# Kernel optimization log

Measured on AMD Instinct MI355X. Metric: run time of the kernel, lower is better.

The kernel has to match this reference:

```python
import jax, jax.numpy as jnp
import numpy as np

R, B, D = 1024, 16, 1024
K_ACTIVE = 20
FB_DECAY = 0.9          # feedback_decay
REFR_W = 1.0            # refractory_weight
FB_W = 0.5              # feedback_weight


def _hex_neighbors(rows=32, cols=32):
    """Toroidal hex grid adjacency: 6 neighbors per region, shape [R, 6]."""
    n = rows * cols
    idx = np.arange(n)
    r, c = idx // cols, idx % cols
    def wrap(rr, cc):
        return (rr % rows) * cols + (cc % cols)
    nbrs = np.stack([
        wrap(r, c - 1), wrap(r, c + 1),
        wrap(r - 1, c), wrap(r + 1, c),
        wrap(r - 1, c + 1), wrap(r + 1, c - 1),
    ], axis=1)
    return nbrs.astype(np.int32)


def setup_inputs() -> dict:
    key = jax.random.key(0)
    k1, k2, k3, k4, k5 = jax.random.split(key, 5)
    return {
        "H": jax.random.normal(k1, (R, B, D), jnp.float32),
        "neighbor_msg": jax.random.normal(k2, (R, B, D), jnp.float32),
        "w": jax.random.normal(k3, (D,), jnp.float32) / np.float32(np.sqrt(D)),
        "theta": jnp.zeros((R,), jnp.float32),
        "refractory": jax.random.uniform(k4, (B, R), jnp.float32),
        "feedback": jax.random.uniform(k5, (B, R), jnp.float32),
        "neighbor_indices": jnp.asarray(_hex_neighbors()),
    }


def _greedy_hex_nms(adj, nbrs, k):
    """adj: [B, R] adjusted scores; nbrs: [R, 6]. Returns hard mask [B, R]."""
    n_regions = adj.shape[1]

    def nms_one(scores):
        order = jnp.argsort(-scores)  # descending

        def step(state, idx):
            sel, sup, cnt = state
            take = (cnt < k) & (~sel[idx]) & (~sup[idx])
            sel = sel.at[idx].set(sel[idx] | take)
            sup = sup.at[idx].set(sup[idx] | take)
            nb = nbrs[idx]  # [6]
            sup = sup.at[nb].set(sup[nb] | take)
            return (sel, sup, cnt + take.astype(jnp.int32)), None

        init = (jnp.zeros(n_regions, bool), jnp.zeros(n_regions, bool), jnp.int32(0))
        (sel, _, _), _ = jax.lax.scan(step, init, order)
        return sel.astype(scores.dtype)

    return jax.vmap(nms_one)(adj)


def reference(H, neighbor_msg, w, theta, refractory, feedback, neighbor_indices):
    # learned score: Linear(D, 1, bias=False) -> [B, R]
    s = jnp.einsum('rbd,d->br', H, w)
    # feedback inhibition from routed message magnitude
    fb_mag = jnp.linalg.norm(neighbor_msg, axis=-1).T          # [B, R]
    fb_new = FB_DECAY * feedback + (1.0 - FB_DECAY) * fb_mag   # updated _feedback
    adj = s - theta[None, :] - REFR_W * refractory - FB_W * fb_new
    hard = jax.lax.stop_gradient(_greedy_hex_nms(adj, neighbor_indices, K_ACTIVE))
    soft = jax.nn.sigmoid(adj)
    ste = hard + soft - jax.lax.stop_gradient(soft)            # straight-through
    Hs = H * ste.T[:, :, None]                                 # [R, B, D]
    return Hs, hard, adj
```

## Files before the change

### kernel.cpp

```cpp
#include <hip/hip_runtime.h>
#include <hip/hip_bf16.h>
#include <math.h>

#define RR 1024
#define BB 16
#define DD 1024
#define K_ACTIVE 20

typedef float vfloat4 __attribute__((ext_vector_type(4)));

__global__ __launch_bounds__(256) void score_kernel(
    const float* __restrict__ H, const float* __restrict__ msg,
    const float* __restrict__ w, const float* __restrict__ theta,
    const float* __restrict__ refr, const float* __restrict__ fb,
    float* __restrict__ adj_out)
{
    const int wave = threadIdx.x >> 6;
    const int lane = threadIdx.x & 63;
    const int pair = blockIdx.x * 4 + wave;
    const int r = pair >> 4;
    const int b = pair & 15;

    const vfloat4* __restrict__ H4 = (const vfloat4*)(H + (size_t)pair * DD);
    const vfloat4* __restrict__ M4 = (const vfloat4*)(msg + (size_t)pair * DD);
    const vfloat4* __restrict__ W4 = (const vfloat4*)w;

    const vfloat4 h0 = H4[lane],       h1 = H4[lane + 64];
    const vfloat4 h2 = H4[lane + 128], h3 = H4[lane + 192];
    const vfloat4 m0 = M4[lane],       m1 = M4[lane + 64];
    const vfloat4 m2 = M4[lane + 128], m3 = M4[lane + 192];
    const vfloat4 w0 = W4[lane],       w1 = W4[lane + 64];
    const vfloat4 w2 = W4[lane + 128], w3 = W4[lane + 192];

    float dot = h0.x * w0.x + h0.y * w0.y + h0.z * w0.z + h0.w * w0.w;
    dot += h1.x * w1.x + h1.y * w1.y + h1.z * w1.z + h1.w * w1.w;
    dot += h2.x * w2.x + h2.y * w2.y + h2.z * w2.z + h2.w * w2.w;
    dot += h3.x * w3.x + h3.y * w3.y + h3.z * w3.z + h3.w * w3.w;

    float ss = m0.x * m0.x + m0.y * m0.y + m0.z * m0.z + m0.w * m0.w;
    ss += m1.x * m1.x + m1.y * m1.y + m1.z * m1.z + m1.w * m1.w;
    ss += m2.x * m2.x + m2.y * m2.y + m2.z * m2.z + m2.w * m2.w;
    ss += m3.x * m3.x + m3.y * m3.y + m3.z * m3.z + m3.w * m3.w;

#pragma unroll
    for (int off = 32; off > 0; off >>= 1) {
        dot += __shfl_down(dot, off);
        ss  += __shfl_down(ss, off);
    }
    if (lane == 0) {
        const float fb_mag = sqrtf(ss);
        const float fb_new = 0.9f * fb[b * RR + r] + 0.1f * fb_mag;
        adj_out[b * RR + r] = dot - theta[r] - refr[b * RR + r] - 0.5f * fb_new;
    }
}

__global__ __launch_bounds__(64) void nms_kernel(
    const float* __restrict__ adj, const int* __restrict__ nbrs,
    float* __restrict__ hard)
{
    __shared__ float val[RR];
    __shared__ int   nb[RR * 6];
    __shared__ unsigned char sel[RR];

    const int b = blockIdx.x;
    const int lane = threadIdx.x;

#pragma unroll
    for (int j = 0; j < 16; ++j) {
        const int i = lane + 64 * j;
        val[i] = adj[b * RR + i];
        sel[i] = 0;
    }
    const int4* nb4g = (const int4*)nbrs;
    int4* nb4s = (int4*)nb;
#pragma unroll
    for (int j = 0; j < 24; ++j)
        nb4s[lane + 64 * j] = nb4g[lane + 64 * j];
    __syncthreads();

    for (int it = 0; it < K_ACTIVE; ++it) {
        float m = -INFINITY;
        int mi = RR;
#pragma unroll
        for (int j = 0; j < 16; ++j) {
            const int i = lane + 64 * j;
            const float v = val[i];
            if (v > m || (v == m && i < mi)) { m = v; mi = i; }
        }
#pragma unroll
        for (int off = 32; off > 0; off >>= 1) {
            const float ov = __shfl_down(m, off);
            const int   oi = __shfl_down(mi, off);
            if (ov > m || (ov == m && oi < mi)) { m = ov; mi = oi; }
        }
        const int   bi = __shfl(mi, 0);
        const float bm = __shfl(m, 0);
        if (bm > -INFINITY) {
            if (lane == 0) { sel[bi] = 1; val[bi] = -INFINITY; }
            if (lane < 6)  { val[nb[bi * 6 + lane]] = -INFINITY; }
        }
        __syncthreads();
    }

#pragma unroll
    for (int j = 0; j < 16; ++j) {
        const int i = lane + 64 * j;
        hard[b * RR + i] = sel[i] ? 1.0f : 0.0f;
    }
}

__global__ __launch_bounds__(256) void gate_kernel(
    const float* __restrict__ H, const float* __restrict__ hard,
    float* __restrict__ Hs)
{
    const int wave = threadIdx.x >> 6;
    const int lane = threadIdx.x & 63;
    const int pair = blockIdx.x * 4 + wave;
    const int r = pair >> 4;
    const int b = pair & 15;
    const float g = hard[b * RR + r];

    vfloat4* out4 = (vfloat4*)(Hs + (size_t)pair * DD);
    if (g != 0.0f) {
        const vfloat4* H4 = (const vfloat4*)(H + (size_t)pair * DD);
        const vfloat4 v0 = H4[lane],       v1 = H4[lane + 64];
        const vfloat4 v2 = H4[lane + 128], v3 = H4[lane + 192];
        __builtin_nontemporal_store(v0, &out4[lane]);
        __builtin_nontemporal_store(v1, &out4[lane + 64]);
        __builtin_nontemporal_store(v2, &out4[lane + 128]);
        __builtin_nontemporal_store(v3, &out4[lane + 192]);
    } else {
        const vfloat4 z = {0.f, 0.f, 0.f, 0.f};
        __builtin_nontemporal_store(z, &out4[lane]);
        __builtin_nontemporal_store(z, &out4[lane + 64]);
        __builtin_nontemporal_store(z, &out4[lane + 128]);
        __builtin_nontemporal_store(z, &out4[lane + 192]);
    }
}

extern "C" void kernel_launch(void* const* d_in, const int* in_sizes, int n_in,
                              void* d_out, int out_size, void* d_ws, size_t ws_size,
                              hipStream_t stream) {
    const float* H     = (const float*)d_in[0];
    const float* msg   = (const float*)d_in[1];
    const float* w     = (const float*)d_in[2];
    const float* theta = (const float*)d_in[3];
    const float* refr  = (const float*)d_in[4];
    const float* fb    = (const float*)d_in[5];
    const int*   nbrs  = (const int*)d_in[6];

    float* out  = (float*)d_out;
    float* Hs   = out;
    float* hard = out + (size_t)RR * BB * DD;
    float* adj  = hard + (size_t)BB * RR;

    score_kernel<<<RR * BB / 4, 256, 0, stream>>>(H, msg, w, theta, refr, fb, adj);
    nms_kernel<<<BB, 64, 0, stream>>>(adj, nbrs, hard);
    gate_kernel<<<RR * BB / 4, 256, 0, stream>>>(H, hard, Hs);
}
```

Baseline: 209.9 us.

## Fuse score, NMS and gate kernels into one persistent kernel with grid barriers

Replaces three kernel launches with a single persistent kernel of 1024 blocks, each wave handling four (r,b) pairs. Software grid barriers built from atomic counters separate the score, NMS and gating phases, and the counters are zeroed by a memset before launch. The aim is to remove launch gaps and the tail of the 16-block NMS kernel. In exchange, the barriers require every block to be co-resident, the grid-wide wait adds overhead, and NMS now reads the neighbour table from global memory instead of shared memory.

```diff
diff --git a/kernel.cpp b/kernel.cpp
--- a/kernel.cpp
+++ b/kernel.cpp
@@ -6,135 +6,138 @@
 #define BB 16
 #define DD 1024
 #define K_ACTIVE 20
+#define NBLK 1024
 
 typedef float vfloat4 __attribute__((ext_vector_type(4)));
 
-__global__ __launch_bounds__(256) void score_kernel(
+__device__ __forceinline__ void grid_sync(int* cnt) {
+    __syncthreads();
+    if (threadIdx.x == 0) {
+        __threadfence();
+        atomicAdd(cnt, 1);
+        while (__hip_atomic_load(cnt, __ATOMIC_RELAXED, __HIP_MEMORY_SCOPE_AGENT) < NBLK)
+            __builtin_amdgcn_s_sleep(1);
+        __threadfence();
+    }
+    __syncthreads();
+}
+
+__global__ __launch_bounds__(256, 4) void fused_kernel(
     const float* __restrict__ H, const float* __restrict__ msg,
     const float* __restrict__ w, const float* __restrict__ theta,
     const float* __restrict__ refr, const float* __restrict__ fb,
-    float* __restrict__ adj_out)
+    const int* __restrict__ nbrs,
+    float* __restrict__ Hs, float* __restrict__ hard, float* __restrict__ adj,
+    int* __restrict__ cnt)
 {
-    const int wave = threadIdx.x >> 6;
+    __shared__ float val[RR];
+    __shared__ unsigned char sel[RR];
+
     const int lane = threadIdx.x & 63;
-    const int pair = blockIdx.x * 4 + wave;
-    const int r = pair >> 4;
-    const int b = pair & 15;
+    const int wgid = (blockIdx.x << 2) + (threadIdx.x >> 6);
 
-    const vfloat4* __restrict__ H4 = (const vfloat4*)(H + (size_t)pair * DD);
-    const vfloat4* __restrict__ M4 = (const vfloat4*)(msg + (size_t)pair * DD);
     const vfloat4* __restrict__ W4 = (const vfloat4*)w;
-
-    const vfloat4 h0 = H4[lane],       h1 = H4[lane + 64];
-    const vfloat4 h2 = H4[lane + 128], h3 = H4[lane + 192];
-    const vfloat4 m0 = M4[lane],       m1 = M4[lane + 64];
-    const vfloat4 m2 = M4[lane + 128], m3 = M4[lane + 192];
     const vfloat4 w0 = W4[lane],       w1 = W4[lane + 64];
     const vfloat4 w2 = W4[lane + 128], w3 = W4[lane + 192];
 
-    float dot = h0.x * w0.x + h0.y * w0.y + h0.z * w0.z + h0.w * w0.w;
-    dot += h1.x * w1.x + h1.y * w1.y + h1.z * w1.z + h1.w * w1.w;
-    dot += h2.x * w2.x + h2.y * w2.y + h2.z * w2.z + h2.w * w2.w;
-    dot += h3.x * w3.x + h3.y * w3.y + h3.z * w3.z + h3.w * w3.w;
+#pragma unroll
+    for (int p = 0; p < 4; ++p) {
+        const int pair = wgid + 4096 * p;
+        const int r = pair >> 4;
+        const int b = pair & 15;
+        const vfloat4* __restrict__ H4 = (const vfloat4*)(H + (size_t)pair * DD);
+        const vfloat4* __restrict__ M4 = (const vfloat4*)(msg + (size_t)pair * DD);
 
-    float ss = m0.x * m0.x + m0.y * m0.y + m0.z * m0.z + m0.w * m0.w;
-    ss += m1.x * m1.x + m1.y * m1.y + m1.z * m1.z + m1.w * m1.w;
-    ss += m2.x * m2.x + m2.y * m2.y + m2.z * m2.z + m2.w * m2.w;
-    ss += m3.x * m3.x + m3.y * m3.y + m3.z * m3.z + m3.w * m3.w;
+        const vfloat4 h0 = H4[lane],       h1 = H4[lane + 64];
+        const vfloat4 h2 = H4[lane + 128], h3 = H4[lane + 192];
+        const vfloat4 m0 = M4[lane],       m1 = M4[lane + 64];
+        const vfloat4 m2 = M4[lane + 128], m3 = M4[lane + 192];
+
+        float dot = h0.x * w0.x + h0.y * w0.y + h0.z * w0.z + h0.w * w0.w;
+        dot += h1.x * w1.x + h1.y * w1.y + h1.z * w1.z + h1.w * w1.w;
+        dot += h2.x * w2.x + h2.y * w2.y + h2.z * w2.z + h2.w * w2.w;
+        dot += h3.x * w3.x + h3.y * w3.y + h3.z * w3.z + h3.w * w3.w;
+
+        float ss = m0.x * m0.x + m0.y * m0.y + m0.z * m0.z + m0.w * m0.w;
+        ss += m1.x * m1.x + m1.y * m1.y + m1.z * m1.z + m1.w * m1.w;
+        ss += m2.x * m2.x + m2.y * m2.y + m2.z * m2.z + m2.w * m2.w;
+        ss += m3.x * m3.x + m3.y * m3.y + m3.z * m3.z + m3.w * m3.w;
 
 #pragma unroll
-    for (int off = 32; off > 0; off >>= 1) {
-        dot += __shfl_down(dot, off);
-        ss  += __shfl_down(ss, off);
+        for (int off = 32; off > 0; off >>= 1) {
+            dot += __shfl_down(dot, off);
+            ss  += __shfl_down(ss, off);
+        }
+        if (lane == 0) {
+            const float fb_mag = sqrtf(ss);
+            const float fb_new = 0.9f * fb[b * RR + r] + 0.1f * fb_mag;
+            adj[b * RR + r] = dot - theta[r] - refr[b * RR + r] - 0.5f * fb_new;
+        }
     }
-    if (lane == 0) {
-        const float fb_mag = sqrtf(ss);
-        const float fb_new = 0.9f * fb[b * RR + r] + 0.1f * fb_mag;
-        adj_out[b * RR + r] = dot - theta[r] - refr[b * RR + r] - 0.5f * fb_new;
-    }
-}
 
-__global__ __launch_bounds__(64) void nms_kernel(
-    const float* __restrict__ adj, const int* __restrict__ nbrs,
-    float* __restrict__ hard)
-{
-    __shared__ float val[RR];
-    __shared__ int   nb[RR * 6];
-    __shared__ unsigned char sel[RR];
+    grid_sync(&cnt[0]);
 
-    const int b = blockIdx.x;
-    const int lane = threadIdx.x;
-
-#pragma unroll
-    for (int j = 0; j < 16; ++j) {
-        const int i = lane + 64 * j;
-        val[i] = adj[b * RR + i];
-        sel[i] = 0;
-    }
-    const int4* nb4g = (const int4*)nbrs;
-    int4* nb4s = (int4*)nb;
-#pragma unroll
-    for (int j = 0; j < 24; ++j)
-        nb4s[lane + 64 * j] = nb4g[lane + 64 * j];
-    __syncthreads();
-
-    for (int it = 0; it < K_ACTIVE; ++it) {
-        float m = -INFINITY;
-        int mi = RR;
+    if (blockIdx.x < BB && threadIdx.x < 64) {
+        const int b = blockIdx.x;
 #pragma unroll
         for (int j = 0; j < 16; ++j) {
             const int i = lane + 64 * j;
-            const float v = val[i];
-            if (v > m || (v == m && i < mi)) { m = v; mi = i; }
+            val[i] = adj[b * RR + i];
+            sel[i] = 0;
+        }
+        for (int it = 0; it < K_ACTIVE; ++it) {
+            float m = -INFINITY;
+            int mi = RR;
+#pragma unroll
+            for (int j = 0; j < 16; ++j) {
+                const int i = lane + 64 * j;
+                const float v = val[i];
+                if (v > m || (v == m && i < mi)) { m = v; mi = i; }
+            }
+#pragma unroll
+            for (int off = 32; off > 0; off >>= 1) {
+                const float ov = __shfl_down(m, off);
+                const int   oi = __shfl_down(mi, off);
+                if (ov > m || (ov == m && oi < mi)) { m = ov; mi = oi; }
+            }
+            const int   bi = __shfl(mi, 0);
+            const float bm = __shfl(m, 0);
+            if (bm > -INFINITY) {
+                if (lane == 0) { sel[bi] = 1; val[bi] = -INFINITY; }
+                if (lane < 6)  { val[nbrs[bi * 6 + lane]] = -INFINITY; }
+            }
         }
 #pragma unroll
-        for (int off = 32; off > 0; off >>= 1) {
-            const float ov = __shfl_down(m, off);
-            const int   oi = __shfl_down(mi, off);
-            if (ov > m || (ov == m && oi < mi)) { m = ov; mi = oi; }
+        for (int j = 0; j < 16; ++j) {
+            const int i = lane + 64 * j;
+            hard[b * RR + i] = sel[i] ? 1.0f : 0.0f;
         }
-        const int   bi = __shfl(mi, 0);
-        const float bm = __shfl(m, 0);
-        if (bm > -INFINITY) {
-            if (lane == 0) { sel[bi] = 1; val[bi] = -INFINITY; }
-            if (lane < 6)  { val[nb[bi * 6 + lane]] = -INFINITY; }
-        }
-        __syncthreads();
     }
 
+    grid_sync(&cnt[1]);
+
 #pragma unroll
-    for (int j = 0; j < 16; ++j) {
-        const int i = lane + 64 * j;
-        hard[b * RR + i] = sel[i] ? 1.0f : 0.0f;
-    }
-}
-
-__global__ __launch_bounds__(256) void gate_kernel(
-    const float* __restrict__ H, const float* __restrict__ hard,
-    float* __restrict__ Hs)
-{
-    const int wave = threadIdx.x >> 6;
-    const int lane = threadIdx.x & 63;
-    const int pair = blockIdx.x * 4 + wave;
-    const int r = pair >> 4;
-    const int b = pair & 15;
-    const float g = hard[b * RR + r];
-
-    vfloat4* out4 = (vfloat4*)(Hs + (size_t)pair * DD);
-    if (g != 0.0f) {
-        const vfloat4* H4 = (const vfloat4*)(H + (size_t)pair * DD);
-        const vfloat4 v0 = H4[lane],       v1 = H4[lane + 64];
-        const vfloat4 v2 = H4[lane + 128], v3 = H4[lane + 192];
-        __builtin_nontemporal_store(v0, &out4[lane]);
-        __builtin_nontemporal_store(v1, &out4[lane + 64]);
-        __builtin_nontemporal_store(v2, &out4[lane + 128]);
-        __builtin_nontemporal_store(v3, &out4[lane + 192]);
-    } else {
-        const vfloat4 z = {0.f, 0.f, 0.f, 0.f};
-        __builtin_nontemporal_store(z, &out4[lane]);
-        __builtin_nontemporal_store(z, &out4[lane + 64]);
-        __builtin_nontemporal_store(z, &out4[lane + 128]);
-        __builtin_nontemporal_store(z, &out4[lane + 192]);
+    for (int p = 0; p < 4; ++p) {
+        const int pair = wgid + 4096 * p;
+        const int r = pair >> 4;
+        const int b = pair & 15;
+        const float g = hard[b * RR + r];
+        vfloat4* out4 = (vfloat4*)(Hs + (size_t)pair * DD);
+        if (g != 0.0f) {
+            const vfloat4* H4 = (const vfloat4*)(H + (size_t)pair * DD);
+            const vfloat4 v0 = H4[lane],       v1 = H4[lane + 64];
+            const vfloat4 v2 = H4[lane + 128], v3 = H4[lane + 192];
+            __builtin_nontemporal_store(v0, &out4[lane]);
+            __builtin_nontemporal_store(v1, &out4[lane + 64]);
+            __builtin_nontemporal_store(v2, &out4[lane + 128]);
+            __builtin_nontemporal_store(v3, &out4[lane + 192]);
+        } else {
+            const vfloat4 z = {0.f, 0.f, 0.f, 0.f};
+            __builtin_nontemporal_store(z, &out4[lane]);
+            __builtin_nontemporal_store(z, &out4[lane + 64]);
+            __builtin_nontemporal_store(z, &out4[lane + 128]);
+            __builtin_nontemporal_store(z, &out4[lane + 192]);
+        }
     }
 }
 
@@ -154,7 +157,7 @@
     float* hard = out + (size_t)RR * BB * DD;
     float* adj  = hard + (size_t)BB * RR;
 
-    score_kernel<<<RR * BB / 4, 256, 0, stream>>>(H, msg, w, theta, refr, fb, adj);
-    nms_kernel<<<BB, 64, 0, stream>>>(adj, nbrs, hard);
-    gate_kernel<<<RR * BB / 4, 256, 0, stream>>>(H, hard, Hs);
+    hipMemsetAsync(d_ws, 0, 16, stream);
+    fused_kernel<<<NBLK, 256, 0, stream>>>(H, msg, w, theta, refr, fb, nbrs,
+                                           Hs, hard, adj, (int*)d_ws);
 }
```

Measured after the change: 415.5 us. +98.0%, slower.

## Use persistent-style grids with software-prefetched rows in score and gate kernels

Applied to the files above, without the earlier changes.

Score and gate kernels now launch 1024 blocks and each wave handles 4 (r,b) rows strided by 4096. The score kernel double-buffers, loading the next row's H and msg while reducing the current one. The gate kernel loads all four gate values up front and switches from nontemporal to normal stores. The aim is more memory-level parallelism and less per-block launch overhead, at the cost of higher register pressure and the loss of the nontemporal store hint.

```diff
diff --git a/kernel.cpp b/kernel.cpp
--- a/kernel.cpp
+++ b/kernel.cpp
@@ -9,7 +9,7 @@
 
 typedef float vfloat4 __attribute__((ext_vector_type(4)));
 
-__global__ __launch_bounds__(256) void score_kernel(
+__global__ __launch_bounds__(256, 4) void score_kernel(
     const float* __restrict__ H, const float* __restrict__ msg,
     const float* __restrict__ w, const float* __restrict__ theta,
     const float* __restrict__ refr, const float* __restrict__ fb,
@@ -17,40 +17,56 @@
 {
     const int wave = threadIdx.x >> 6;
     const int lane = threadIdx.x & 63;
-    const int pair = blockIdx.x * 4 + wave;
-    const int r = pair >> 4;
-    const int b = pair & 15;
+    const int wid  = blockIdx.x * 4 + wave;
 
-    const vfloat4* __restrict__ H4 = (const vfloat4*)(H + (size_t)pair * DD);
-    const vfloat4* __restrict__ M4 = (const vfloat4*)(msg + (size_t)pair * DD);
     const vfloat4* __restrict__ W4 = (const vfloat4*)w;
-
-    const vfloat4 h0 = H4[lane],       h1 = H4[lane + 64];
-    const vfloat4 h2 = H4[lane + 128], h3 = H4[lane + 192];
-    const vfloat4 m0 = M4[lane],       m1 = M4[lane + 64];
-    const vfloat4 m2 = M4[lane + 128], m3 = M4[lane + 192];
     const vfloat4 w0 = W4[lane],       w1 = W4[lane + 64];
     const vfloat4 w2 = W4[lane + 128], w3 = W4[lane + 192];
 
-    float dot = h0.x * w0.x + h0.y * w0.y + h0.z * w0.z + h0.w * w0.w;
-    dot += h1.x * w1.x + h1.y * w1.y + h1.z * w1.z + h1.w * w1.w;
-    dot += h2.x * w2.x + h2.y * w2.y + h2.z * w2.z + h2.w * w2.w;
-    dot += h3.x * w3.x + h3.y * w3.y + h3.z * w3.z + h3.w * w3.w;
-
-    float ss = m0.x * m0.x + m0.y * m0.y + m0.z * m0.z + m0.w * m0.w;
-    ss += m1.x * m1.x + m1.y * m1.y + m1.z * m1.z + m1.w * m1.w;
-    ss += m2.x * m2.x + m2.y * m2.y + m2.z * m2.z + m2.w * m2.w;
-    ss += m3.x * m3.x + m3.y * m3.y + m3.z * m3.z + m3.w * m3.w;
+    int pair = wid;
+    const vfloat4* __restrict__ H4 = (const vfloat4*)(H + (size_t)pair * DD);
+    const vfloat4* __restrict__ M4 = (const vfloat4*)(msg + (size_t)pair * DD);
+    vfloat4 ha0 = H4[lane], ha1 = H4[lane + 64], ha2 = H4[lane + 128], ha3 = H4[lane + 192];
+    vfloat4 ma0 = M4[lane], ma1 = M4[lane + 64], ma2 = M4[lane + 128], ma3 = M4[lane + 192];
 
 #pragma unroll
-    for (int off = 32; off > 0; off >>= 1) {
-        dot += __shfl_down(dot, off);
-        ss  += __shfl_down(ss, off);
-    }
-    if (lane == 0) {
-        const float fb_mag = sqrtf(ss);
-        const float fb_new = 0.9f * fb[b * RR + r] + 0.1f * fb_mag;
-        adj_out[b * RR + r] = dot - theta[r] - refr[b * RR + r] - 0.5f * fb_new;
+    for (int p = 0; p < 4; ++p) {
+        vfloat4 hb0 = {0,0,0,0}, hb1 = {0,0,0,0}, hb2 = {0,0,0,0}, hb3 = {0,0,0,0};
+        vfloat4 mb0 = {0,0,0,0}, mb1 = {0,0,0,0}, mb2 = {0,0,0,0}, mb3 = {0,0,0,0};
+        if (p < 3) {
+            const int npair = pair + 4096;
+            const vfloat4* __restrict__ Hn = (const vfloat4*)(H + (size_t)npair * DD);
+            const vfloat4* __restrict__ Mn = (const vfloat4*)(msg + (size_t)npair * DD);
+            hb0 = Hn[lane]; hb1 = Hn[lane + 64]; hb2 = Hn[lane + 128]; hb3 = Hn[lane + 192];
+            mb0 = Mn[lane]; mb1 = Mn[lane + 64]; mb2 = Mn[lane + 128]; mb3 = Mn[lane + 192];
+        }
+
+        float dot = ha0.x * w0.x + ha0.y * w0.y + ha0.z * w0.z + ha0.w * w0.w;
+        dot += ha1.x * w1.x + ha1.y * w1.y + ha1.z * w1.z + ha1.w * w1.w;
+        dot += ha2.x * w2.x + ha2.y * w2.y + ha2.z * w2.z + ha2.w * w2.w;
+        dot += ha3.x * w3.x + ha3.y * w3.y + ha3.z * w3.z + ha3.w * w3.w;
+
+        float ss = ma0.x * ma0.x + ma0.y * ma0.y + ma0.z * ma0.z + ma0.w * ma0.w;
+        ss += ma1.x * ma1.x + ma1.y * ma1.y + ma1.z * ma1.z + ma1.w * ma1.w;
+        ss += ma2.x * ma2.x + ma2.y * ma2.y + ma2.z * ma2.z + ma2.w * ma2.w;
+        ss += ma3.x * ma3.x + ma3.y * ma3.y + ma3.z * ma3.z + ma3.w * ma3.w;
+
+#pragma unroll
+        for (int off = 32; off > 0; off >>= 1) {
+            dot += __shfl_down(dot, off);
+            ss  += __shfl_down(ss, off);
+        }
+        if (lane == 0) {
+            const int r = pair >> 4;
+            const int b = pair & 15;
+            const float fb_mag = sqrtf(ss);
+            const float fb_new = 0.9f * fb[b * RR + r] + 0.1f * fb_mag;
+            adj_out[b * RR + r] = dot - theta[r] - refr[b * RR + r] - 0.5f * fb_new;
+        }
+
+        ha0 = hb0; ha1 = hb1; ha2 = hb2; ha3 = hb3;
+        ma0 = mb0; ma1 = mb1; ma2 = mb2; ma3 = mb3;
+        pair += 4096;
     }
 }
 
@@ -109,32 +125,40 @@
     }
 }
 
-__global__ __launch_bounds__(256) void gate_kernel(
+__global__ __launch_bounds__(256, 4) void gate_kernel(
     const float* __restrict__ H, const float* __restrict__ hard,
     float* __restrict__ Hs)
 {
     const int wave = threadIdx.x >> 6;
     const int lane = threadIdx.x & 63;
-    const int pair = blockIdx.x * 4 + wave;
-    const int r = pair >> 4;
-    const int b = pair & 15;
-    const float g = hard[b * RR + r];
+    const int wid  = blockIdx.x * 4 + wave;
 
-    vfloat4* out4 = (vfloat4*)(Hs + (size_t)pair * DD);
-    if (g != 0.0f) {
-        const vfloat4* H4 = (const vfloat4*)(H + (size_t)pair * DD);
-        const vfloat4 v0 = H4[lane],       v1 = H4[lane + 64];
-        const vfloat4 v2 = H4[lane + 128], v3 = H4[lane + 192];
-        __builtin_nontemporal_store(v0, &out4[lane]);
-        __builtin_nontemporal_store(v1, &out4[lane + 64]);
-        __builtin_nontemporal_store(v2, &out4[lane + 128]);
-        __builtin_nontemporal_store(v3, &out4[lane + 192]);
-    } else {
-        const vfloat4 z = {0.f, 0.f, 0.f, 0.f};
-        __builtin_nontemporal_store(z, &out4[lane]);
-        __builtin_nontemporal_store(z, &out4[lane + 64]);
-        __builtin_nontemporal_store(z, &out4[lane + 128]);
-        __builtin_nontemporal_store(z, &out4[lane + 192]);
+    float g[4];
+#pragma unroll
+    for (int p = 0; p < 4; ++p) {
+        const int pair = wid + 4096 * p;
+        g[p] = hard[(pair & 15) * RR + (pair >> 4)];
+    }
+
+#pragma unroll
+    for (int p = 0; p < 4; ++p) {
+        const int pair = wid + 4096 * p;
+        vfloat4* out4 = (vfloat4*)(Hs + (size_t)pair * DD);
+        if (g[p] != 0.0f) {
+            const vfloat4* __restrict__ H4 = (const vfloat4*)(H + (size_t)pair * DD);
+            const vfloat4 v0 = H4[lane],       v1 = H4[lane + 64];
+            const vfloat4 v2 = H4[lane + 128], v3 = H4[lane + 192];
+            out4[lane]       = v0;
+            out4[lane + 64]  = v1;
+            out4[lane + 128] = v2;
+            out4[lane + 192] = v3;
+        } else {
+            const vfloat4 z = {0.f, 0.f, 0.f, 0.f};
+            out4[lane]       = z;
+            out4[lane + 64]  = z;
+            out4[lane + 128] = z;
+            out4[lane + 192] = z;
+        }
     }
 }
 
@@ -154,7 +178,7 @@
     float* hard = out + (size_t)RR * BB * DD;
     float* adj  = hard + (size_t)BB * RR;
 
-    score_kernel<<<RR * BB / 4, 256, 0, stream>>>(H, msg, w, theta, refr, fb, adj);
+    score_kernel<<<1024, 256, 0, stream>>>(H, msg, w, theta, refr, fb, adj);
     nms_kernel<<<BB, 64, 0, stream>>>(adj, nbrs, hard);
-    gate_kernel<<<RR * BB / 4, 256, 0, stream>>>(H, hard, Hs);
+    gate_kernel<<<1024, 256, 0, stream>>>(H, hard, Hs);
 }
```

Result: no change. 212.5 us (+1.2%).

## Zero output with memset and scatter only selected rows instead of full gate pass

Applied to the files above, without the earlier changes.

Writing the gated output is split in two: an async memset zeroes all of Hs, and a new scatter kernel with one 64-thread block per (r,b) copies H only for selected pairs, exiting early otherwise. The aim is to avoid re-reading H for the roughly 98% of unselected rows and to let the memset run as a fast fill path. The score kernel also gains an occupancy hint and a scheduling barrier after its loads. The cost is 16K tiny blocks launched mostly to exit at once, plus an extra memset operation in the stream.

```diff
diff --git a/kernel.cpp b/kernel.cpp
--- a/kernel.cpp
+++ b/kernel.cpp
@@ -9,7 +9,7 @@
 
 typedef float vfloat4 __attribute__((ext_vector_type(4)));
 
-__global__ __launch_bounds__(256) void score_kernel(
+__global__ __launch_bounds__(256, 4) void score_kernel(
     const float* __restrict__ H, const float* __restrict__ msg,
     const float* __restrict__ w, const float* __restrict__ theta,
     const float* __restrict__ refr, const float* __restrict__ fb,
@@ -31,6 +31,8 @@
     const vfloat4 m2 = M4[lane + 128], m3 = M4[lane + 192];
     const vfloat4 w0 = W4[lane],       w1 = W4[lane + 64];
     const vfloat4 w2 = W4[lane + 128], w3 = W4[lane + 192];
+
+    __builtin_amdgcn_sched_barrier(0);
 
     float dot = h0.x * w0.x + h0.y * w0.y + h0.z * w0.z + h0.w * w0.w;
     dot += h1.x * w1.x + h1.y * w1.y + h1.z * w1.z + h1.w * w1.w;
@@ -109,33 +111,24 @@
     }
 }
 
-__global__ __launch_bounds__(256) void gate_kernel(
+__global__ __launch_bounds__(64) void scatter_kernel(
     const float* __restrict__ H, const float* __restrict__ hard,
     float* __restrict__ Hs)
 {
-    const int wave = threadIdx.x >> 6;
-    const int lane = threadIdx.x & 63;
-    const int pair = blockIdx.x * 4 + wave;
+    const int pair = blockIdx.x;
     const int r = pair >> 4;
     const int b = pair & 15;
-    const float g = hard[b * RR + r];
+    if (hard[b * RR + r] == 0.0f) return;
 
+    const int lane = threadIdx.x;
+    const vfloat4* __restrict__ H4 = (const vfloat4*)(H + (size_t)pair * DD);
     vfloat4* out4 = (vfloat4*)(Hs + (size_t)pair * DD);
-    if (g != 0.0f) {
-        const vfloat4* H4 = (const vfloat4*)(H + (size_t)pair * DD);
-        const vfloat4 v0 = H4[lane],       v1 = H4[lane + 64];
-        const vfloat4 v2 = H4[lane + 128], v3 = H4[lane + 192];
-        __builtin_nontemporal_store(v0, &out4[lane]);
-        __builtin_nontemporal_store(v1, &out4[lane + 64]);
-        __builtin_nontemporal_store(v2, &out4[lane + 128]);
-        __builtin_nontemporal_store(v3, &out4[lane + 192]);
-    } else {
-        const vfloat4 z = {0.f, 0.f, 0.f, 0.f};
-        __builtin_nontemporal_store(z, &out4[lane]);
-        __builtin_nontemporal_store(z, &out4[lane + 64]);
-        __builtin_nontemporal_store(z, &out4[lane + 128]);
-        __builtin_nontemporal_store(z, &out4[lane + 192]);
-    }
+    const vfloat4 v0 = H4[lane],       v1 = H4[lane + 64];
+    const vfloat4 v2 = H4[lane + 128], v3 = H4[lane + 192];
+    out4[lane]       = v0;
+    out4[lane + 64]  = v1;
+    out4[lane + 128] = v2;
+    out4[lane + 192] = v3;
 }
 
 extern "C" void kernel_launch(void* const* d_in, const int* in_sizes, int n_in,
@@ -154,7 +147,9 @@
     float* hard = out + (size_t)RR * BB * DD;
     float* adj  = hard + (size_t)BB * RR;
 
+    hipMemsetAsync(Hs, 0, (size_t)RR * BB * DD * sizeof(float), stream);
+
     score_kernel<<<RR * BB / 4, 256, 0, stream>>>(H, msg, w, theta, refr, fb, adj);
     nms_kernel<<<BB, 64, 0, stream>>>(adj, nbrs, hard);
-    gate_kernel<<<RR * BB / 4, 256, 0, stream>>>(H, hard, Hs);
+    scatter_kernel<<<RR * BB, 64, 0, stream>>>(H, hard, Hs);
 }
```

Result: slower. 217.3 us (+3.5%).
